# Kernel tuning notes

Hardware: AMD Instinct MI355X
Metric: run time of the kernel (lower is better)

Reference implementation:

```python
import jax, jax.numpy as jnp
import numpy as np

N_NODES = 8192
N_EDGES = 262144
N_REL = 8
NUM_CLASSES = 151
EMB = 256
BOX = 1024
HID = 512
OUT = 256
N_TASKS = 2


def setup_inputs() -> dict:
    key = jax.random.key(0)
    ks = jax.random.split(key, 20)
    w = lambda k, shape: jax.random.normal(k, shape, dtype=jnp.float32) * 0.02
    return {
        "box_features": jax.random.normal(ks[0], (N_NODES, BOX), dtype=jnp.float32),
        "pred_labels": jax.random.randint(ks[1], (N_NODES,), 0, NUM_CLASSES),
        "edge_index": jax.random.randint(ks[2], (2, N_EDGES), 0, N_NODES),
        "edge_type": jax.random.randint(ks[3], (N_EDGES,), 0, N_REL),
        "nodes_per_graph": 128,
        "emb_table": w(ks[4], (NUM_CLASSES, EMB)),
        "W_lin": w(ks[5], (BOX + EMB, HID)),
        "b_lin": jnp.zeros((HID,), jnp.float32),
        "rel_W1": w(ks[6], (N_REL, HID, HID)),
        "root_W1": w(ks[7], (HID, HID)),
        "b1": jnp.zeros((HID,), jnp.float32),
        "rel_W2": w(ks[8], (N_REL, HID, OUT)),
        "root_W2": w(ks[9], (HID, OUT)),
        "b2": jnp.zeros((OUT,), jnp.float32),
        "Wc1": w(ks[10], (OUT, OUT)),
        "bc1": jnp.zeros((OUT,), jnp.float32),
        "Wc2": w(ks[11], (OUT, N_TASKS)),
        "bc2": jnp.zeros((N_TASKS,), jnp.float32),
    }


def rgcn_conv(x, src, dst, etype, rel_W, root_W, b):
    """PyG RGCNConv: per-relation mean aggregation + root weight + bias."""
    R, _, out_dim = rel_W.shape
    N = x.shape[0]
    transformed = jnp.einsum('ni,rio->rno', x, rel_W)      # [R, N, out]
    msg = transformed[etype, src]                           # [E, out] gather per edge
    seg = etype * N + dst                                   # (relation, dst) segment id
    sums = jax.ops.segment_sum(msg, seg, num_segments=R * N)
    cnt = jax.ops.segment_sum(jnp.ones((msg.shape[0],), x.dtype), seg, num_segments=R * N)
    mean = sums / jnp.maximum(cnt, 1.0)[:, None]
    agg = mean.reshape(R, N, out_dim).sum(0)                # sum over relations
    return agg + x @ root_W + b


def reference(box_features, pred_labels, edge_index, edge_type, nodes_per_graph,
              emb_table, W_lin, b_lin, rel_W1, root_W1, b1, rel_W2, root_W2, b2,
              Wc1, bc1, Wc2, bc2):
    src, dst = edge_index[0], edge_index[1]
    # obj embedding + concat with box features
    x = jnp.concatenate([box_features, emb_table[pred_labels]], axis=-1)  # [N, 1280]
    x = x @ W_lin + b_lin                                                  # [N, 512]
    x = jax.nn.relu(rgcn_conv(x, src, dst, edge_type, rel_W1, root_W1, b1))
    x = rgcn_conv(x, src, dst, edge_type, rel_W2, root_W2, b2)             # [N, 256]
    # mean graph pooling over equal-size graphs
    B = x.shape[0] // nodes_per_graph
    pooled = x.reshape(B, nodes_per_graph, -1).mean(axis=1)                # [B, 256]
    # classifier (dropout is identity in eval)
    y_logits = (pooled @ Wc1 + bc1) @ Wc2 + bc2                            # [B, n_tasks]
    y_prob = jax.nn.softmax(y_logits, axis=-1)
    return y_logits, y_prob
```

## Files before the change

kernel.cpp:

```cpp
#include <hip/hip_runtime.h>
#include <cstdint>

#define NNODES 8192
#define NEDGES 262144
#define NRELS  8
#define EMBD   256
#define BOXD   1024
#define HIDD   512
#define OUTD   256
#define NSEG   (NRELS * NNODES)
#define K0DIM  (BOXD + EMBD)
#define KSDIM  (NRELS * HIDD + HIDD)

using bf16x8 = __attribute__((ext_vector_type(8))) short;
using f32x4  = __attribute__((ext_vector_type(4))) float;
using us4    = __attribute__((ext_vector_type(4))) unsigned short;

__device__ __forceinline__ unsigned short f2b(float f) {
    union { float f; uint32_t u; } v; v.f = f;
    uint32_t r = v.u + 0x7FFFu + ((v.u >> 16) & 1u);
    return (unsigned short)(r >> 16);
}

__device__ __forceinline__ us4 cvt4(f32x4 v) {
    us4 u;
    u[0] = f2b(v[0]); u[1] = f2b(v[1]); u[2] = f2b(v[2]); u[3] = f2b(v[3]);
    return u;
}

__device__ __forceinline__ float b2f_lo(uint32_t w) {
    union { uint32_t u; float f; } v; v.u = w << 16; return v.f;
}
__device__ __forceinline__ float b2f_hi(uint32_t w) {
    union { uint32_t u; float f; } v; v.u = w & 0xffff0000u; return v.f;
}

__global__ void k_build_x0(const float* __restrict__ box, const int* __restrict__ labels,
                           const float* __restrict__ emb, unsigned short* __restrict__ X0) {
    int n = blockIdx.x;
    int lab = labels[n];
    const f32x4* b = (const f32x4*)(box + (size_t)n * BOXD);
    const f32x4* e = (const f32x4*)(emb + (size_t)lab * EMBD);
    us4* o = (us4*)(X0 + (size_t)n * K0DIM);
    for (int j = threadIdx.x; j < K0DIM / 4; j += 256) {
        f32x4 v = (j < BOXD / 4) ? b[j] : e[j - BOXD / 4];
        o[j] = cvt4(v);
    }
}

__global__ void k_transpose_all(const float* __restrict__ W_lin, const float* __restrict__ rel_W1,
                                const float* __restrict__ root_W1,
                                unsigned short* __restrict__ W0t, unsigned short* __restrict__ W1t) {
    __shared__ float t[32][33];
    int bid = blockIdx.x;
    const float* src; unsigned short* dst; int No, ld, kOff, kb, ob;
    if (bid < 640)        { int g = bid;        src = W_lin;   dst = W0t; No = 512; ld = K0DIM; kOff = 0;    kb = g % 40;  ob = g / 40; }
    else if (bid < 2688)  { int g = bid - 640;  src = rel_W1;  dst = W1t; No = 512; ld = KSDIM; kOff = 0;    kb = g % 128; ob = g / 128; }
    else                  { int g = bid - 2688; src = root_W1; dst = W1t; No = 512; ld = KSDIM; kOff = 4096; kb = g % 16;  ob = g / 16; }
    int kt = kb * 32, ot = ob * 32;
    int tx = threadIdx.x & 31, ty = threadIdx.x >> 5;
#pragma unroll
    for (int i = 0; i < 4; i++) {
        int k = kt + ty + i * 8;
        t[ty + i * 8][tx] = src[(size_t)k * No + ot + tx];
    }
    __syncthreads();
#pragma unroll
    for (int i = 0; i < 4; i++) {
        int o = ot + ty + i * 8;
        dst[(size_t)o * ld + kOff + kt + tx] = f2b(t[tx][ty + i * 8]);
    }
}

__global__ void k_wc12(const float* __restrict__ Wc1, const float* __restrict__ bc1,
                       const float* __restrict__ Wc2, const float* __restrict__ bc2,
                       const float* __restrict__ b2, float* __restrict__ Wsmall,
                       float* __restrict__ bbig) {
    __shared__ float r0[256], r1[256];
    int i = threadIdx.x;
    float w0 = 0.f, w1 = 0.f;
    for (int o = 0; o < 256; o++) {
        float c = Wc1[i * 256 + o];
        w0 += c * Wc2[o * 2 + 0];
        w1 += c * Wc2[o * 2 + 1];
    }
    Wsmall[i * 2 + 0] = w0;
    Wsmall[i * 2 + 1] = w1;
    r0[i] = b2[i] * w0 + bc1[i] * Wc2[i * 2 + 0];
    r1[i] = b2[i] * w1 + bc1[i] * Wc2[i * 2 + 1];
    __syncthreads();
    for (int s = 128; s > 0; s >>= 1) {
        if (i < s) { r0[i] += r0[i + s]; r1[i] += r1[i + s]; }
        __syncthreads();
    }
    if (i == 0) { bbig[0] = r0[0] + bc2[0]; bbig[1] = r1[0] + bc2[1]; }
}

__global__ void k_wbig(const float* __restrict__ rel_W2, const float* __restrict__ root_W2,
                       const float* __restrict__ Wsmall, float* __restrict__ Wbig) {
    int k = blockIdx.x * 256 + threadIdx.x;
    const float* row = (k < 4096) ? rel_W2 + (size_t)k * 256
                                  : root_W2 + (size_t)(k - 4096) * 256;
    float s0 = 0.f, s1 = 0.f;
    for (int o = 0; o < 256; o++) {
        float v = row[o];
        s0 += v * Wsmall[o * 2 + 0];
        s1 += v * Wsmall[o * 2 + 1];
    }
    Wbig[k * 2 + 0] = s0;
    Wbig[k * 2 + 1] = s1;
}

__global__ void k_hist(const int* __restrict__ etype, const int* __restrict__ edst,
                       int* __restrict__ cnt) {
    int e = blockIdx.x * 256 + threadIdx.x;
    if (e >= NEDGES) return;
    atomicAdd(&cnt[etype[e] * NNODES + edst[e]], 1);
}

__global__ __launch_bounds__(1024) void k_scan(const int* __restrict__ cnt,
                                               int* __restrict__ segstart) {
    __shared__ int part[1024];
    __shared__ int sup[16];
    __shared__ int supx[16];
    int t = threadIdx.x;
    int base = t * 64;
    int s = 0;
    for (int i = 0; i < 64; i++) s += cnt[base + i];
    part[t] = s;
    __syncthreads();
    if (t < 16) {
        int a = 0;
        for (int i = 0; i < 64; i++) a += part[t * 64 + i];
        sup[t] = a;
    }
    __syncthreads();
    if (t == 0) {
        int a = 0;
        for (int i = 0; i < 16; i++) { supx[i] = a; a += sup[i]; }
    }
    __syncthreads();
    int a = supx[t >> 6];
    for (int i = (t & ~63); i < t; i++) a += part[i];
    for (int i = 0; i < 64; i++) { segstart[base + i] = a; a += cnt[base + i]; }
    if (t == 1023) segstart[NSEG] = a;
}

__global__ void k_scatter(const int* __restrict__ etype, const int* __restrict__ esrc,
                          const int* __restrict__ edst, const int* __restrict__ segstart,
                          int* __restrict__ cursor, int* __restrict__ esorted) {
    int e = blockIdx.x * 256 + threadIdx.x;
    if (e >= NEDGES) return;
    int key = etype[e] * NNODES + edst[e];
    int pos = atomicAdd(&cursor[key], 1);
    esorted[segstart[key] + pos] = esrc[e];
}

__global__ __launch_bounds__(256) void k_aggregate(
        const unsigned short* __restrict__ x, const int* __restrict__ segstart,
        const int* __restrict__ esorted, unsigned short* __restrict__ Xin) {
    int seg = blockIdx.x * 4 + (threadIdx.x >> 6);
    int lane = threadIdx.x & 63;
    int r = seg >> 13;
    int dstn = seg & (NNODES - 1);
    float a[8] = {0, 0, 0, 0, 0, 0, 0, 0};
    float b[8] = {0, 0, 0, 0, 0, 0, 0, 0};
    int s0 = segstart[seg], s1 = segstart[seg + 1];
    int t = s0;
    for (; t + 2 <= s1; t += 2) {
        uint4 v0 = *(const uint4*)(x + (size_t)esorted[t] * HIDD + lane * 8);
        uint4 v1 = *(const uint4*)(x + (size_t)esorted[t + 1] * HIDD + lane * 8);
        a[0] += b2f_lo(v0.x); a[1] += b2f_hi(v0.x);
        a[2] += b2f_lo(v0.y); a[3] += b2f_hi(v0.y);
        a[4] += b2f_lo(v0.z); a[5] += b2f_hi(v0.z);
        a[6] += b2f_lo(v0.w); a[7] += b2f_hi(v0.w);
        b[0] += b2f_lo(v1.x); b[1] += b2f_hi(v1.x);
        b[2] += b2f_lo(v1.y); b[3] += b2f_hi(v1.y);
        b[4] += b2f_lo(v1.z); b[5] += b2f_hi(v1.z);
        b[6] += b2f_lo(v1.w); b[7] += b2f_hi(v1.w);
    }
    if (t < s1) {
        uint4 v0 = *(const uint4*)(x + (size_t)esorted[t] * HIDD + lane * 8);
        a[0] += b2f_lo(v0.x); a[1] += b2f_hi(v0.x);
        a[2] += b2f_lo(v0.y); a[3] += b2f_hi(v0.y);
        a[4] += b2f_lo(v0.z); a[5] += b2f_hi(v0.z);
        a[6] += b2f_lo(v0.w); a[7] += b2f_hi(v0.w);
    }
    float iv = (s1 > s0) ? (1.0f / (float)(s1 - s0)) : 1.0f;
#pragma unroll
    for (int j = 0; j < 8; j++) a[j] = (a[j] + b[j]) * iv;
    uint4 u;
    u.x = (uint32_t)f2b(a[0]) | ((uint32_t)f2b(a[1]) << 16);
    u.y = (uint32_t)f2b(a[2]) | ((uint32_t)f2b(a[3]) << 16);
    u.z = (uint32_t)f2b(a[4]) | ((uint32_t)f2b(a[5]) << 16);
    u.w = (uint32_t)f2b(a[6]) | ((uint32_t)f2b(a[7]) << 16);
    *(uint4*)(Xin + (size_t)dstn * KSDIM + r * HIDD + lane * 8) = u;
}

__global__ __launch_bounds__(256) void k_aggpool(
        const unsigned short* __restrict__ x, const int* __restrict__ segstart,
        const int* __restrict__ esorted, float* __restrict__ PXp) {
    int b = blockIdx.x;
    int q = b & 3, r = (b >> 2) & 7, g = b >> 5;
    int wave = threadIdx.x >> 6, lane = threadIdx.x & 63;
    float a[8] = {0, 0, 0, 0, 0, 0, 0, 0};
    int segbase = r * NNODES + g * 128 + q * 32 + wave * 8;
#pragma unroll 1
    for (int i = 0; i < 8; ++i) {
        int s0 = segstart[segbase + i], s1 = segstart[segbase + i + 1];
        if (s0 == s1) continue;
        float p[8] = {0, 0, 0, 0, 0, 0, 0, 0};
        for (int t = s0; t < s1; ++t) {
            uint4 v = *(const uint4*)(x + (size_t)esorted[t] * HIDD + lane * 8);
            p[0] += b2f_lo(v.x); p[1] += b2f_hi(v.x);
            p[2] += b2f_lo(v.y); p[3] += b2f_hi(v.y);
            p[4] += b2f_lo(v.z); p[5] += b2f_hi(v.z);
            p[6] += b2f_lo(v.w); p[7] += b2f_hi(v.w);
        }
        float w = 1.0f / (128.0f * (float)(s1 - s0));
#pragma unroll
        for (int j = 0; j < 8; j++) a[j] += p[j] * w;
    }
    __shared__ float red[4][512];
#pragma unroll
    for (int j = 0; j < 8; j++) red[wave][lane * 8 + j] = a[j];
    __syncthreads();
    for (int c = threadIdx.x; c < 512; c += 256) {
        float s = red[0][c] + red[1][c] + red[2][c] + red[3][c];
        PXp[((size_t)q * 64 + g) * KSDIM + r * 512 + c] = s;
    }
}

__global__ __launch_bounds__(256) void k_rootpool(
        const unsigned short* __restrict__ x, float* __restrict__ PXp) {
    int g = blockIdx.x >> 2, q = blockIdx.x & 3;
    int wave = threadIdx.x >> 6, lane = threadIdx.x & 63;
    float a[8] = {0, 0, 0, 0, 0, 0, 0, 0};
    int n0 = g * 128 + q * 32 + wave * 8;
#pragma unroll
    for (int i = 0; i < 8; ++i) {
        uint4 v = *(const uint4*)(x + (size_t)(n0 + i) * HIDD + lane * 8);
        a[0] += b2f_lo(v.x); a[1] += b2f_hi(v.x);
        a[2] += b2f_lo(v.y); a[3] += b2f_hi(v.y);
        a[4] += b2f_lo(v.z); a[5] += b2f_hi(v.z);
        a[6] += b2f_lo(v.w); a[7] += b2f_hi(v.w);
    }
    __shared__ float red[4][512];
#pragma unroll
    for (int j = 0; j < 8; j++) red[wave][lane * 8 + j] = a[j];
    __syncthreads();
    for (int c = threadIdx.x; c < 512; c += 256) {
        float s = red[0][c] + red[1][c] + red[2][c] + red[3][c];
        PXp[((size_t)q * 64 + g) * KSDIM + 4096 + c] = s * (1.0f / 128.0f);
    }
}

__global__ __launch_bounds__(512, 4) void k_gemm(
        const unsigned short* __restrict__ A,
        const unsigned short* __restrict__ Bt,
        float* __restrict__ P,
        int M, int N, int K, int Kc) {
    __shared__ unsigned short As[2][128 * 64];
    __shared__ unsigned short Bs[2][128 * 64];
    const int tid = threadIdx.x;
    const int lane = tid & 63, wid = tid >> 6;
    const int tiles_m = M >> 7;
    const int tm = blockIdx.x % tiles_m, tn = blockIdx.x / tiles_m;
    const int m0 = tm << 7, n0 = tn << 7;
    const int wr = wid >> 2, wc = wid & 3;
    const int k0 = blockIdx.y * Kc;

    f32x4 acc[4][2];
#pragma unroll
    for (int i = 0; i < 4; i++)
#pragma unroll
        for (int j = 0; j < 2; j++) acc[i][j] = (f32x4){0.f, 0.f, 0.f, 0.f};

    const int rowg = tid >> 3;
    const int srcc = (tid & 7) ^ (rowg & 7);
    const unsigned short* gA = A  + (size_t)(m0 + rowg) * K + k0 + srcc * 8;
    const unsigned short* gB = Bt + (size_t)(n0 + rowg) * K + k0 + srcc * 8;
    const int ldsbase = wid * 512;

    auto stage = [&](int bsel, int kt) {
#pragma unroll
        for (int i = 0; i < 2; ++i) {
            __builtin_amdgcn_global_load_lds(
                (const __attribute__((address_space(1))) void*)(gA + kt + i * 64 * K),
                (__attribute__((address_space(3))) void*)&As[bsel][i * 4096 + ldsbase], 16, 0, 0);
            __builtin_amdgcn_global_load_lds(
                (const __attribute__((address_space(1))) void*)(gB + kt + i * 64 * K),
                (__attribute__((address_space(3))) void*)&Bs[bsel][i * 4096 + ldsbase], 16, 0, 0);
        }
    };

    const int arow = wr * 64 + (lane & 15);
    const int brow = wc * 32 + (lane & 15);
    const int l7 = lane & 7;
    const int c0 = lane >> 4;

    const int nt = Kc >> 6;
    int cur = 0;
    stage(0, 0);
    asm volatile("s_waitcnt vmcnt(0)" ::: "memory");
    __builtin_amdgcn_s_barrier();

    for (int t = 0; t < nt; ++t) {
        if (t + 1 < nt) stage(cur ^ 1, (t + 1) * 64);
#pragma unroll
        for (int s4 = 0; s4 < 2; ++s4) {
            const int slot = (c0 + s4 * 4) ^ l7;
            bf16x8 af[4], bfr[2];
#pragma unroll
            for (int m = 0; m < 4; m++)
                af[m] = *(const bf16x8*)&As[cur][(arow + m * 16) * 64 + slot * 8];
#pragma unroll
            for (int n = 0; n < 2; n++)
                bfr[n] = *(const bf16x8*)&Bs[cur][(brow + n * 16) * 64 + slot * 8];
#pragma unroll
            for (int m = 0; m < 4; m++)
#pragma unroll
                for (int n = 0; n < 2; n++)
                    acc[m][n] = __builtin_amdgcn_mfma_f32_16x16x32_bf16(af[m], bfr[n], acc[m][n], 0, 0, 0);
        }
        if (t + 1 < nt) {
            asm volatile("s_waitcnt vmcnt(0)" ::: "memory");
            __builtin_amdgcn_s_barrier();
            cur ^= 1;
        }
    }

    float* Pout = P + (size_t)blockIdx.y * M * N;
    const int crow0 = m0 + wr * 64 + (lane >> 4) * 4;
    const int ccol0 = n0 + wc * 32 + (lane & 15);
#pragma unroll
    for (int n = 0; n < 2; n++) {
        int col = ccol0 + n * 16;
#pragma unroll
        for (int m = 0; m < 4; m++)
#pragma unroll
            for (int r = 0; r < 4; r++)
                Pout[(size_t)(crow0 + m * 16 + r) * N + col] = acc[m][n][r];
    }
}

template <int RELU, int WROOT>
__global__ void k_reduce_bf(const float* __restrict__ P, const float* __restrict__ bias,
                            unsigned short* __restrict__ xbf, unsigned short* __restrict__ Xin,
                            int MN) {
    int idx = (blockIdx.x * 256 + threadIdx.x) * 4;
    f32x4 v = *(const f32x4*)&P[idx];
    v += *(const f32x4*)&P[(size_t)MN + idx];
    v += *(const f32x4*)&bias[idx & 511];
    if (RELU) {
#pragma unroll
        for (int j = 0; j < 4; j++) v[j] = fmaxf(v[j], 0.f);
    }
    us4 u = cvt4(v);
    *(us4*)&xbf[idx] = u;
    if (WROOT) {
        int row = idx >> 9, col = idx & 511;
        *(us4*)&Xin[(size_t)row * KSDIM + NRELS * HIDD + col] = u;
    }
}

__global__ void k_logits(const float* __restrict__ PXp, const float* __restrict__ Wbig,
                         const float* __restrict__ bbig, float* __restrict__ out) {
    __shared__ float r0[256], r1[256];
    int g = blockIdx.x, tid = threadIdx.x;
    const float* p0 = PXp + ((size_t)0 * 64 + g) * KSDIM;
    const float* p1 = PXp + ((size_t)1 * 64 + g) * KSDIM;
    const float* p2 = PXp + ((size_t)2 * 64 + g) * KSDIM;
    const float* p3 = PXp + ((size_t)3 * 64 + g) * KSDIM;
    float s0 = 0.f, s1 = 0.f;
#pragma unroll
    for (int i = 0; i < 18; i++) {
        int k = i * 256 + tid;
        float px = p0[k] + p1[k] + p2[k] + p3[k];
        s0 += px * Wbig[k * 2 + 0];
        s1 += px * Wbig[k * 2 + 1];
    }
    r0[tid] = s0; r1[tid] = s1;
    __syncthreads();
    for (int s = 128; s > 0; s >>= 1) {
        if (tid < s) { r0[tid] += r0[tid + s]; r1[tid] += r1[tid + s]; }
        __syncthreads();
    }
    if (tid == 0) {
        float l0 = r0[0] + bbig[0], l1 = r1[0] + bbig[1];
        out[g * 2 + 0] = l0;
        out[g * 2 + 1] = l1;
        float m = fmaxf(l0, l1);
        float e0 = expf(l0 - m), e1 = expf(l1 - m);
        float inv = 1.0f / (e0 + e1);
        out[128 + g * 2 + 0] = e0 * inv;
        out[128 + g * 2 + 1] = e1 * inv;
    }
}

extern "C" void kernel_launch(void* const* d_in, const int* in_sizes, int n_in,
                              void* d_out, int out_size, void* d_ws, size_t ws_size,
                              hipStream_t stream) {
    const float* box     = (const float*)d_in[0];
    const int*   labels  = (const int*)d_in[1];
    const int*   eidx    = (const int*)d_in[2];
    const int*   etype   = (const int*)d_in[3];
    const float* emb     = (const float*)d_in[5];
    const float* W_lin   = (const float*)d_in[6];
    const float* b_lin   = (const float*)d_in[7];
    const float* rel_W1  = (const float*)d_in[8];
    const float* root_W1 = (const float*)d_in[9];
    const float* b1      = (const float*)d_in[10];
    const float* rel_W2  = (const float*)d_in[11];
    const float* root_W2 = (const float*)d_in[12];
    const float* b2      = (const float*)d_in[13];
    const float* Wc1     = (const float*)d_in[14];
    const float* bc1     = (const float*)d_in[15];
    const float* Wc2     = (const float*)d_in[16];
    const float* bc2     = (const float*)d_in[17];
    const int* esrc = eidx;
    const int* edst = eidx + NEDGES;

    char* ws = (char*)d_ws;
    size_t off = 0;
    auto alloc = [&](size_t bytes) -> char* {
        char* p = ws + off;
        off += (bytes + 255) & ~(size_t)255;
        return p;
    };
    float* Pp = (float*)alloc((size_t)2 * NNODES * HIDD * 4);
    unsigned short* Xin = (unsigned short*)alloc((size_t)NNODES * KSDIM * 2);
    unsigned short* X0  = Xin;
    unsigned short* xbf = (unsigned short*)alloc((size_t)NNODES * HIDD * 2);
    unsigned short* W0t = (unsigned short*)alloc((size_t)HIDD * K0DIM * 2);
    unsigned short* W1t = (unsigned short*)alloc((size_t)HIDD * KSDIM * 2);
    float* PXp    = (float*)alloc((size_t)4 * 64 * KSDIM * 4);
    float* Wsmall = (float*)alloc((size_t)256 * 2 * 4);
    float* Wbig   = (float*)alloc((size_t)KSDIM * 2 * 4);
    float* bbig   = (float*)alloc(2 * 4);
    int*   cnt     = (int*)alloc((size_t)NSEG * 4);
    int*   cursor  = (int*)alloc((size_t)NSEG * 4);
    int*   segst   = (int*)alloc((size_t)(NSEG + 1) * 4);
    int*   esorted = (int*)alloc((size_t)NEDGES * 4);
    if (off > ws_size) return;

    float* out = (float*)d_out;
    const int MN = NNODES * HIDD;

    hipMemsetAsync(cnt, 0, (size_t)2 * NSEG * 4, stream);
    k_build_x0<<<NNODES, 256, 0, stream>>>(box, labels, emb, X0);
    k_transpose_all<<<2944, 256, 0, stream>>>(W_lin, rel_W1, root_W1, W0t, W1t);
    k_wc12<<<1, 256, 0, stream>>>(Wc1, bc1, Wc2, bc2, b2, Wsmall, bbig);
    k_wbig<<<KSDIM / 256, 256, 0, stream>>>(rel_W2, root_W2, Wsmall, Wbig);
    k_hist<<<NEDGES / 256, 256, 0, stream>>>(etype, edst, cnt);
    k_scan<<<1, 1024, 0, stream>>>(cnt, segst);
    k_scatter<<<NEDGES / 256, 256, 0, stream>>>(etype, esrc, edst, segst, cursor, esorted);

    k_gemm<<<dim3((NNODES / 128) * (HIDD / 128), 2), 512, 0, stream>>>(
        X0, W0t, Pp, NNODES, HIDD, K0DIM, K0DIM / 2);
    k_reduce_bf<0, 1><<<MN / 1024, 256, 0, stream>>>(Pp, b_lin, xbf, Xin, MN);

    k_aggregate<<<NSEG / 4, 256, 0, stream>>>(xbf, segst, esorted, Xin);
    k_gemm<<<dim3((NNODES / 128) * (HIDD / 128), 2), 512, 0, stream>>>(
        Xin, W1t, Pp, NNODES, HIDD, KSDIM, KSDIM / 2);
    k_reduce_bf<1, 0><<<MN / 1024, 256, 0, stream>>>(Pp, b1, xbf, Xin, MN);

    k_aggpool<<<2048, 256, 0, stream>>>(xbf, segst, esorted, PXp);
    k_rootpool<<<256, 256, 0, stream>>>(xbf, PXp);
    k_logits<<<64, 256, 0, stream>>>(PXp, Wbig, bbig, out);
}
```

Measured before the change: 255.4 us.

## Parallelize segment scan across blocks and split gather kernels into column halves

Replaces the single-block 1024-thread prefix scan with a two-kernel multi-block scan (per-block reductions, then a per-block exclusive scan). Splits the edge gather in k_aggregate and k_aggpool into two launches, each covering 256 of the 512 feature columns with 8-byte loads, so that the gathered working set of x per pass is halved and fits better in cache. The aggregate loop is also unrolled by four edges. In exchange it adds two extra launches and reads the edge index lists twice.

```diff
diff --git a/kernel.cpp b/kernel.cpp
--- a/kernel.cpp
+++ b/kernel.cpp
@@ -118,32 +118,43 @@
     atomicAdd(&cnt[etype[e] * NNODES + edst[e]], 1);
 }
 
-__global__ __launch_bounds__(1024) void k_scan(const int* __restrict__ cnt,
-                                               int* __restrict__ segstart) {
-    __shared__ int part[1024];
-    __shared__ int sup[16];
-    __shared__ int supx[16];
-    int t = threadIdx.x;
-    int base = t * 64;
-    int s = 0;
-    for (int i = 0; i < 64; i++) s += cnt[base + i];
-    part[t] = s;
-    __syncthreads();
-    if (t < 16) {
-        int a = 0;
-        for (int i = 0; i < 64; i++) a += part[t * 64 + i];
-        sup[t] = a;
-    }
-    __syncthreads();
-    if (t == 0) {
-        int a = 0;
-        for (int i = 0; i < 16; i++) { supx[i] = a; a += sup[i]; }
-    }
-    __syncthreads();
-    int a = supx[t >> 6];
-    for (int i = (t & ~63); i < t; i++) a += part[i];
-    for (int i = 0; i < 64; i++) { segstart[base + i] = a; a += cnt[base + i]; }
-    if (t == 1023) segstart[NSEG] = a;
+__global__ void k_scan1(const int* __restrict__ cnt, int* __restrict__ bsum) {
+    __shared__ int red[256];
+    int b = blockIdx.x, t = threadIdx.x;
+    red[t] = cnt[b * 256 + t];
+    __syncthreads();
+    for (int s = 128; s > 0; s >>= 1) {
+        if (t < s) red[t] += red[t + s];
+        __syncthreads();
+    }
+    if (t == 0) bsum[b] = red[0];
+}
+
+__global__ void k_scan2(const int* __restrict__ cnt, const int* __restrict__ bsum,
+                        int* __restrict__ segstart) {
+    __shared__ int buf[256];
+    int b = blockIdx.x, t = threadIdx.x;
+    buf[t] = bsum[t];
+    __syncthreads();
+    for (int o = 1; o < 256; o <<= 1) {
+        int x = (t >= o) ? buf[t - o] : 0;
+        __syncthreads();
+        buf[t] += x;
+        __syncthreads();
+    }
+    int base = (b == 0) ? 0 : buf[b - 1];
+    __syncthreads();
+    int v = cnt[b * 256 + t];
+    buf[t] = v;
+    __syncthreads();
+    for (int o = 1; o < 256; o <<= 1) {
+        int x = (t >= o) ? buf[t - o] : 0;
+        __syncthreads();
+        buf[t] += x;
+        __syncthreads();
+    }
+    segstart[b * 256 + t] = base + buf[t] - v;
+    if (b == 255 && t == 255) segstart[NSEG] = base + buf[t];
 }
 
 __global__ void k_scatter(const int* __restrict__ etype, const int* __restrict__ esrc,
@@ -158,76 +169,68 @@
 
 __global__ __launch_bounds__(256) void k_aggregate(
         const unsigned short* __restrict__ x, const int* __restrict__ segstart,
-        const int* __restrict__ esorted, unsigned short* __restrict__ Xin) {
+        const int* __restrict__ esorted, unsigned short* __restrict__ Xin, int colOff) {
     int seg = blockIdx.x * 4 + (threadIdx.x >> 6);
     int lane = threadIdx.x & 63;
     int r = seg >> 13;
     int dstn = seg & (NNODES - 1);
-    float a[8] = {0, 0, 0, 0, 0, 0, 0, 0};
-    float b[8] = {0, 0, 0, 0, 0, 0, 0, 0};
+    const unsigned short* xc = x + colOff + lane * 4;
+    float a[4] = {0, 0, 0, 0};
     int s0 = segstart[seg], s1 = segstart[seg + 1];
     int t = s0;
-    for (; t + 2 <= s1; t += 2) {
-        uint4 v0 = *(const uint4*)(x + (size_t)esorted[t] * HIDD + lane * 8);
-        uint4 v1 = *(const uint4*)(x + (size_t)esorted[t + 1] * HIDD + lane * 8);
+    for (; t + 4 <= s1; t += 4) {
+        uint2 v0 = *(const uint2*)(xc + (size_t)esorted[t] * HIDD);
+        uint2 v1 = *(const uint2*)(xc + (size_t)esorted[t + 1] * HIDD);
+        uint2 v2 = *(const uint2*)(xc + (size_t)esorted[t + 2] * HIDD);
+        uint2 v3 = *(const uint2*)(xc + (size_t)esorted[t + 3] * HIDD);
+        a[0] += b2f_lo(v0.x) + b2f_lo(v1.x) + b2f_lo(v2.x) + b2f_lo(v3.x);
+        a[1] += b2f_hi(v0.x) + b2f_hi(v1.x) + b2f_hi(v2.x) + b2f_hi(v3.x);
+        a[2] += b2f_lo(v0.y) + b2f_lo(v1.y) + b2f_lo(v2.y) + b2f_lo(v3.y);
+        a[3] += b2f_hi(v0.y) + b2f_hi(v1.y) + b2f_hi(v2.y) + b2f_hi(v3.y);
+    }
+    for (; t < s1; ++t) {
+        uint2 v0 = *(const uint2*)(xc + (size_t)esorted[t] * HIDD);
         a[0] += b2f_lo(v0.x); a[1] += b2f_hi(v0.x);
         a[2] += b2f_lo(v0.y); a[3] += b2f_hi(v0.y);
-        a[4] += b2f_lo(v0.z); a[5] += b2f_hi(v0.z);
-        a[6] += b2f_lo(v0.w); a[7] += b2f_hi(v0.w);
-        b[0] += b2f_lo(v1.x); b[1] += b2f_hi(v1.x);
-        b[2] += b2f_lo(v1.y); b[3] += b2f_hi(v1.y);
-        b[4] += b2f_lo(v1.z); b[5] += b2f_hi(v1.z);
-        b[6] += b2f_lo(v1.w); b[7] += b2f_hi(v1.w);
-    }
-    if (t < s1) {
-        uint4 v0 = *(const uint4*)(x + (size_t)esorted[t] * HIDD + lane * 8);
-        a[0] += b2f_lo(v0.x); a[1] += b2f_hi(v0.x);
-        a[2] += b2f_lo(v0.y); a[3] += b2f_hi(v0.y);
-        a[4] += b2f_lo(v0.z); a[5] += b2f_hi(v0.z);
-        a[6] += b2f_lo(v0.w); a[7] += b2f_hi(v0.w);
     }
     float iv = (s1 > s0) ? (1.0f / (float)(s1 - s0)) : 1.0f;
-#pragma unroll
-    for (int j = 0; j < 8; j++) a[j] = (a[j] + b[j]) * iv;
-    uint4 u;
-    u.x = (uint32_t)f2b(a[0]) | ((uint32_t)f2b(a[1]) << 16);
-    u.y = (uint32_t)f2b(a[2]) | ((uint32_t)f2b(a[3]) << 16);
-    u.z = (uint32_t)f2b(a[4]) | ((uint32_t)f2b(a[5]) << 16);
-    u.w = (uint32_t)f2b(a[6]) | ((uint32_t)f2b(a[7]) << 16);
-    *(uint4*)(Xin + (size_t)dstn * KSDIM + r * HIDD + lane * 8) = u;
+    uint2 u;
+    u.x = (uint32_t)f2b(a[0] * iv) | ((uint32_t)f2b(a[1] * iv) << 16);
+    u.y = (uint32_t)f2b(a[2] * iv) | ((uint32_t)f2b(a[3] * iv) << 16);
+    *(uint2*)(Xin + (size_t)dstn * KSDIM + r * HIDD + colOff + lane * 4) = u;
 }
 
 __global__ __launch_bounds__(256) void k_aggpool(
         const unsigned short* __restrict__ x, const int* __restrict__ segstart,
-        const int* __restrict__ esorted, float* __restrict__ PXp) {
+        const int* __restrict__ esorted, float* __restrict__ PXp, int colOff) {
     int b = blockIdx.x;
     int q = b & 3, r = (b >> 2) & 7, g = b >> 5;
     int wave = threadIdx.x >> 6, lane = threadIdx.x & 63;
-    float a[8] = {0, 0, 0, 0, 0, 0, 0, 0};
+    const unsigned short* xc = x + colOff + lane * 4;
+    float a[4] = {0, 0, 0, 0};
     int segbase = r * NNODES + g * 128 + q * 32 + wave * 8;
 #pragma unroll 1
     for (int i = 0; i < 8; ++i) {
         int s0 = segstart[segbase + i], s1 = segstart[segbase + i + 1];
         if (s0 == s1) continue;
-        float p[8] = {0, 0, 0, 0, 0, 0, 0, 0};
+        float p[4] = {0, 0, 0, 0};
         for (int t = s0; t < s1; ++t) {
-            uint4 v = *(const uint4*)(x + (size_t)esorted[t] * HIDD + lane * 8);
+            uint2 v = *(const uint2*)(xc + (size_t)esorted[t] * HIDD);
             p[0] += b2f_lo(v.x); p[1] += b2f_hi(v.x);
             p[2] += b2f_lo(v.y); p[3] += b2f_hi(v.y);
-            p[4] += b2f_lo(v.z); p[5] += b2f_hi(v.z);
-            p[6] += b2f_lo(v.w); p[7] += b2f_hi(v.w);
         }
         float w = 1.0f / (128.0f * (float)(s1 - s0));
 #pragma unroll
-        for (int j = 0; j < 8; j++) a[j] += p[j] * w;
-    }
-    __shared__ float red[4][512];
-#pragma unroll
-    for (int j = 0; j < 8; j++) red[wave][lane * 8 + j] = a[j];
-    __syncthreads();
-    for (int c = threadIdx.x; c < 512; c += 256) {
+        for (int j = 0; j < 4; j++) a[j] += p[j] * w;
+    }
+    __shared__ float red[4][256];
+#pragma unroll
+    for (int j = 0; j < 4; j++) red[wave][lane * 4 + j] = a[j];
+    __syncthreads();
+    if (threadIdx.x < 256) {
+        int c = threadIdx.x;
         float s = red[0][c] + red[1][c] + red[2][c] + red[3][c];
-        PXp[((size_t)q * 64 + g) * KSDIM + r * 512 + c] = s;
+        PXp[((size_t)q * 64 + g) * KSDIM + r * 512 + colOff + c] = s;
     }
 }
 
@@ -441,6 +444,7 @@
     int*   cnt     = (int*)alloc((size_t)NSEG * 4);
     int*   cursor  = (int*)alloc((size_t)NSEG * 4);
     int*   segst   = (int*)alloc((size_t)(NSEG + 1) * 4);
+    int*   bsum    = (int*)alloc((size_t)256 * 4);
     int*   esorted = (int*)alloc((size_t)NEDGES * 4);
     if (off > ws_size) return;
 
@@ -453,19 +457,22 @@
     k_wc12<<<1, 256, 0, stream>>>(Wc1, bc1, Wc2, bc2, b2, Wsmall, bbig);
     k_wbig<<<KSDIM / 256, 256, 0, stream>>>(rel_W2, root_W2, Wsmall, Wbig);
     k_hist<<<NEDGES / 256, 256, 0, stream>>>(etype, edst, cnt);
-    k_scan<<<1, 1024, 0, stream>>>(cnt, segst);
+    k_scan1<<<256, 256, 0, stream>>>(cnt, bsum);
+    k_scan2<<<256, 256, 0, stream>>>(cnt, bsum, segst);
     k_scatter<<<NEDGES / 256, 256, 0, stream>>>(etype, esrc, edst, segst, cursor, esorted);
 
     k_gemm<<<dim3((NNODES / 128) * (HIDD / 128), 2), 512, 0, stream>>>(
         X0, W0t, Pp, NNODES, HIDD, K0DIM, K0DIM / 2);
     k_reduce_bf<0, 1><<<MN / 1024, 256, 0, stream>>>(Pp, b_lin, xbf, Xin, MN);
 
-    k_aggregate<<<NSEG / 4, 256, 0, stream>>>(xbf, segst, esorted, Xin);
+    k_aggregate<<<NSEG / 4, 256, 0, stream>>>(xbf, segst, esorted, Xin, 0);
+    k_aggregate<<<NSEG / 4, 256, 0, stream>>>(xbf, segst, esorted, Xin, 256);
     k_gemm<<<dim3((NNODES / 128) * (HIDD / 128), 2), 512, 0, stream>>>(
         Xin, W1t, Pp, NNODES, HIDD, KSDIM, KSDIM / 2);
     k_reduce_bf<1, 0><<<MN / 1024, 256, 0, stream>>>(Pp, b1, xbf, Xin, MN);
 
-    k_aggpool<<<2048, 256, 0, stream>>>(xbf, segst, esorted, PXp);
+    k_aggpool<<<2048, 256, 0, stream>>>(xbf, segst, esorted, PXp, 0);
+    k_aggpool<<<2048, 256, 0, stream>>>(xbf, segst, esorted, PXp, 256);
     k_rootpool<<<256, 256, 0, stream>>>(xbf, PXp);
     k_logits<<<64, 256, 0, stream>>>(PXp, Wbig, bbig, out);
 }
```

Result: slower. 263.6 us (+3.2%).
